# Optimization experiments

Hardware: AMD Instinct MI355X
Metric: run time of the kernel (lower is better)

## Reference

```python
import jax, jax.numpy as jnp
import numpy as np


def setup_inputs() -> dict:
    key = jax.random.key(0)
    ks = jax.random.split(key, 12)
    B, N, D_in, D = 64, 512, 512, 512
    inp = {
        "x": jax.random.normal(ks[0], (B, N, D_in), dtype=jnp.float32),
        "adj": jax.random.uniform(ks[1], (B, N, N), dtype=jnp.float32),
        "mask": jnp.ones((B, N, 1), dtype=jnp.float32),
        "W_enc": jax.random.normal(ks[2], (D_in, D), dtype=jnp.float32) * (1.0 / np.sqrt(D_in)),
        "b_enc": jnp.zeros((D,), dtype=jnp.float32),
        "Wz": jax.random.normal(ks[3], (D, D), dtype=jnp.float32) * (1.0 / np.sqrt(D)),
        "Uz": jax.random.normal(ks[4], (D, D), dtype=jnp.float32) * (1.0 / np.sqrt(D)),
        "bz": jnp.zeros((D,), dtype=jnp.float32),
        "Wr": jax.random.normal(ks[5], (D, D), dtype=jnp.float32) * (1.0 / np.sqrt(D)),
        "Ur": jax.random.normal(ks[6], (D, D), dtype=jnp.float32) * (1.0 / np.sqrt(D)),
        "br": jnp.zeros((D,), dtype=jnp.float32),
        "Wh": jax.random.normal(ks[7], (D, D), dtype=jnp.float32) * (1.0 / np.sqrt(D)),
        "Uh": jax.random.normal(ks[8], (D, D), dtype=jnp.float32) * (1.0 / np.sqrt(D)),
        "bh": jnp.zeros((D,), dtype=jnp.float32),
        "ba": jnp.zeros((D,), dtype=jnp.float32),
        "steps": 2,
    }
    return inp


def _gru_step(h, adj, mask, Wz, Uz, bz, Wr, Ur, br, Wh, Uh, bh, ba, act):
    # aggregated neighbor messages: [B,N,D]
    a = jnp.einsum('bnm,bmd->bnd', adj, h) + ba
    z = act(a @ Wz + h @ Uz + bz)          # update gate
    r = act(a @ Wr + h @ Ur + br)          # reset gate
    hc = jnp.tanh(a @ Wh + (r * h) @ Uh + bh)
    hc = hc * mask
    return (1.0 - z) * h + z * hc


def reference(x, adj, mask, W_enc, b_enc, Wz, Uz, bz, Wr, Ur, br, Wh, Uh, bh, ba, steps):
    act = jax.nn.relu
    h = mask * act(x @ W_enc + b_enc)      # [B,N,D]
    for _ in range(steps):
        h = _gru_step(h, adj, mask, Wz, Uz, bz, Wr, Ur, br, Wh, Uh, bh, ba, act)
    return h
```

## Files before the change

kernel.cpp:

```cpp
#include <hip/hip_runtime.h>


#define LD 512
#define NN ((long)LD * LD)

typedef unsigned short u16;
typedef _Float16 f16;
typedef f16 f16x8 __attribute__((ext_vector_type(8)));
typedef float f32x4 __attribute__((ext_vector_type(4)));

__device__ __forceinline__ u16 f2h(float f) { f16 h = (f16)f; return *(u16*)&h; }
__device__ __forceinline__ float h2f(u16 b) { f16 h = *(f16*)&b; return (float)h; }

__device__ __forceinline__ void gload16(const void* g, void* l) {
  __builtin_amdgcn_global_load_lds(
      (const __attribute__((address_space(1))) void*)g,
      (__attribute__((address_space(3))) void*)l, 16, 0, 0);
}

__global__ void cvt_f16(const float* __restrict__ in, u16* __restrict__ out, int n4) {
  int i = blockIdx.x * blockDim.x + threadIdx.x;
  if (i >= n4) return;
  float4 v = reinterpret_cast<const float4*>(in)[i];
  ushort4 o;
  o.x = f2h(v.x); o.y = f2h(v.y); o.z = f2h(v.z); o.w = f2h(v.w);
  reinterpret_cast<ushort4*>(out)[i] = o;
}

__global__ void cvt2h(const float* __restrict__ in, u16* __restrict__ ohi,
                      u16* __restrict__ olo, int n4) {
  int i = blockIdx.x * blockDim.x + threadIdx.x;
  if (i >= n4) return;
  float4 v = reinterpret_cast<const float4*>(in)[i];
  ushort4 h, l;
  h.x = f2h(v.x); l.x = f2h(v.x - h2f(h.x));
  h.y = f2h(v.y); l.y = f2h(v.y - h2f(h.y));
  h.z = f2h(v.z); l.z = f2h(v.z - h2f(h.z));
  h.w = f2h(v.w); l.w = f2h(v.w - h2f(h.w));
  reinterpret_cast<ushort4*>(ohi)[i] = h;
  reinterpret_cast<ushort4*>(olo)[i] = l;
}

__global__ void wconv1(const float* __restrict__ in, u16* __restrict__ out, float scale) {
  __shared__ float sm[32][33];
  int tx = threadIdx.x & 31, ty = threadIdx.x >> 5;
  int k0 = blockIdx.y * 32, n0 = blockIdx.x * 32;
#pragma unroll
  for (int i = 0; i < 32; i += 8)
    sm[ty + i][tx] = in[(size_t)(k0 + ty + i) * LD + n0 + tx];
  __syncthreads();
#pragma unroll
  for (int i = 0; i < 32; i += 8)
    out[(size_t)(n0 + ty + i) * LD + k0 + tx] = f2h(sm[tx][ty + i] * scale);
}

__global__ void wconv2h(const float* __restrict__ in, u16* __restrict__ ohi,
                        u16* __restrict__ olo, float scale) {
  __shared__ float sm[32][33];
  int tx = threadIdx.x & 31, ty = threadIdx.x >> 5;
  int k0 = blockIdx.y * 32, n0 = blockIdx.x * 32;
#pragma unroll
  for (int i = 0; i < 32; i += 8)
    sm[ty + i][tx] = in[(size_t)(k0 + ty + i) * LD + n0 + tx];
  __syncthreads();
#pragma unroll
  for (int i = 0; i < 32; i += 8) {
    float v = sm[tx][ty + i] * scale;
    u16 hi = f2h(v);
    size_t o = (size_t)(n0 + ty + i) * LD + k0 + tx;
    ohi[o] = hi;
    olo[o] = f2h(v - h2f(hi));
  }
}

__global__ void transp16(const u16* __restrict__ in, u16* __restrict__ out) {
  __shared__ u16 sm[64][65];
  int b = blockIdx.z;
  int n0 = blockIdx.y * 64, d0 = blockIdx.x * 64;
  int lane = threadIdx.x & 63, grp = threadIdx.x >> 6;
  const u16* src = in + ((size_t)b * LD + n0) * LD + d0;
#pragma unroll
  for (int i = grp; i < 64; i += 4)
    sm[i][lane] = src[(size_t)i * LD + lane];
  __syncthreads();
  u16* dst = out + ((size_t)b * LD + d0) * LD + n0;
#pragma unroll
  for (int i = grp; i < 64; i += 4)
    dst[(size_t)i * LD + lane] = sm[lane][i];
}

struct PENC {
  static constexpr int P = 3;
  static constexpr int AI[3] = {0, 1, 1}, BI[3] = {0, 0, 1};
  static constexpr int SA[3] = {1, 1, 0}, SB[3] = {1, 0, 1};
};
struct PA {
  static constexpr int P = 1;
  static constexpr int AI[1] = {0}, BI[1] = {0};
  static constexpr int SA[1] = {1}, SB[1] = {1};
};
struct PZ {
  static constexpr int P = 2;
  static constexpr int AI[2] = {0, 1}, BI[2] = {0, 1};
  static constexpr int SA[2] = {1, 1}, SB[2] = {1, 1};
};
struct PR {
  static constexpr int P = 4;
  static constexpr int AI[4] = {0, 0, 1, 2}, BI[4] = {0, 1, 1, 2};
  static constexpr int SA[4] = {1, 0, 1, 1}, SB[4] = {1, 1, 0, 1};
};
struct PG1 {
  static constexpr int P = 6;
  static constexpr int AI[6] = {0, 0, 1, 2, 3, 3}, BI[6] = {0, 1, 1, 2, 2, 3};
  static constexpr int SA[6] = {1, 0, 1, 1, 1, 0}, SB[6] = {1, 1, 0, 1, 0, 1};
};
struct PG2 {
  static constexpr int P = 2;
  static constexpr int AI[2] = {0, 1}, BI[2] = {0, 1};
  static constexpr int SA[2] = {1, 1}, SB[2] = {1, 1};
};

struct Desc {
  const u16* Aop[4];
  const u16* Bop[4];
  const float* bias1;
  const float* mask;
  const float* hf32;
  const u16* z16;
  float* outf;
  u16* o16;
  u16* o16b;
};

template <int EPI, class PL>
__global__ __launch_bounds__(512, 4) void gemmf(Desc d) {
  __shared__ __align__(16) u16 As[2][8192];
  __shared__ __align__(16) u16 Bs[2][4096];

  const int t = threadIdx.x;
  const int lane = t & 63;
  const int wid = t >> 6;
  const int wr = wid >> 1, wc = wid & 1;

  const int id = (int)blockIdx.x;
  const int swz = (id & 7) * 64 + (id >> 3);
  const int colb = swz & 3;
  const int rowb = swz >> 2;
  size_t baseA, baseB;
  int rowBase0;
  if (EPI == 1) {
    const int by2 = rowb & 1;
    const size_t bz = (size_t)(rowb >> 1);
    baseA = bz * NN + (size_t)by2 * 256 * LD;
    baseB = bz * NN + (size_t)colb * 128 * LD;
    rowBase0 = (int)bz * 512 + by2 * 256;
  } else {
    baseA = (size_t)rowb * 256 * LD;
    baseB = (size_t)colb * 128 * LD;
    rowBase0 = rowb * 256;
  }

  auto stageA = [&](const u16* Aop, int kb, u16* dst) {
#pragma unroll
    for (int s = 0; s < 2; ++s) {
      const int r = s * 128 + (t >> 2), c = t & 3;
      const int g = c ^ (r & 3) ^ ((r >> 2) & 3);
      gload16(Aop + baseA + (size_t)r * LD + kb + g * 8, dst + s * 4096 + t * 8);
    }
  };
  auto stageB = [&](const u16* Bop, int kb, u16* dst) {
    const int r = t >> 2, c = t & 3;
    const int g = c ^ (r & 3) ^ ((r >> 2) & 3);
    gload16(Bop + baseB + (size_t)r * LD + kb + g * 8, dst + t * 8);
  };

  const int lk = lane >> 4;
  const int RA = wr * 64 + (lane & 15);
  const int RB = wc * 64 + (lane & 15);
  const int offA = RA * 32 + ((lk ^ ((RA & 3) ^ ((RA >> 2) & 3))) * 8);
  const int offB = RB * 32 + ((lk ^ ((RB & 3) ^ ((RB >> 2) & 3))) * 8);

  f32x4 acc[4][4] = {};

  stageA(d.Aop[PL::AI[0]], 0, As[0]);
  stageB(d.Bop[PL::BI[0]], 0, Bs[0]);
  asm volatile("s_waitcnt vmcnt(0)" ::: "memory");
  __builtin_amdgcn_s_barrier();

  int aS = 0, bS = 0;
  for (int kk = 0; kk < 16; ++kk) {
#pragma unroll
    for (int p = 0; p < PL::P; ++p) {
      f16x8 af[4], bf[4];
#pragma unroll
      for (int i = 0; i < 4; ++i) af[i] = *(const f16x8*)&As[aS][offA + i * 512];
#pragma unroll
      for (int j = 0; j < 4; ++j) bf[j] = *(const f16x8*)&Bs[bS][offB + j * 512];
      const int np = (p + 1 == PL::P) ? 0 : p + 1;
      const int nkb = (p + 1 == PL::P) ? (kk + 1) * 32 : kk * 32;
      const bool last = (kk == 15) && (p == PL::P - 1);
      if (!last) {
        if (PL::SA[np]) stageA(d.Aop[PL::AI[np]], nkb, As[aS ^ 1]);
        if (PL::SB[np]) stageB(d.Bop[PL::BI[np]], nkb, Bs[bS ^ 1]);
      }
      __builtin_amdgcn_s_setprio(1);
#pragma unroll
      for (int i = 0; i < 4; ++i)
#pragma unroll
        for (int j = 0; j < 4; ++j)
          acc[i][j] = __builtin_amdgcn_mfma_f32_16x16x32_f16(af[i], bf[j], acc[i][j], 0, 0, 0);
      __builtin_amdgcn_s_setprio(0);
      __syncthreads();
      if (!last) {
        aS ^= PL::SA[np];
        bS ^= PL::SB[np];
      }
    }
  }

  const float S4 = 0.0625f;
  const float S12 = 2.44140625e-4f;
  const int rowBase = rowBase0 + wr * 64 + (lane >> 4) * 4;
  const int colBase = colb * 128 + wc * 64 + (lane & 15);
#pragma unroll
  for (int i = 0; i < 4; ++i) {
#pragma unroll
    for (int j = 0; j < 4; ++j) {
      const int col = colBase + j * 16;
      const float bv = d.bias1[col];
#pragma unroll
      for (int r = 0; r < 4; ++r) {
        const int row = rowBase + i * 16 + r;
        const size_t idx = (size_t)row * LD + col;
        const float a = acc[i][j][r];
        if (EPI == 0) {
          float v = fmaxf(a + bv, 0.0f) * d.mask[row];
          d.outf[idx] = v;
          d.o16[idx] = f2h(v * S4);
        } else if (EPI == 1) {
          float v = a + bv * S4;
          u16 hi = f2h(v);
          d.o16[idx] = hi;
          d.o16b[idx] = f2h(v - h2f(hi));
        } else if (EPI == 2) {
          float v = fmaxf(a + bv, 0.0f);
          d.o16[idx] = f2h(v * S4);
        } else if (EPI == 3) {
          float v = fmaxf(a + bv, 0.0f) * d.hf32[idx];
          u16 hi = f2h(v * S12);
          d.o16[idx] = hi;
          float rec = h2f(hi) * 4096.0f;
          d.o16b[idx] = f2h((v - rec) * S12);
        } else {
          float hc = tanhf(a + bv) * d.mask[row];
          float z = 16.0f * h2f(d.z16[idx]);
          float h = d.hf32[idx];
          float hn = (1.0f - z) * h + z * hc;
          d.outf[idx] = hn;
          d.o16[idx] = f2h(hn * S4);
        }
      }
    }
  }
}

extern "C" void kernel_launch(void* const* d_in, const int* in_sizes, int n_in,
                              void* d_out, int out_size, void* d_ws, size_t ws_size,
                              hipStream_t stream) {
  const float* x    = (const float*)d_in[0];
  const float* adj  = (const float*)d_in[1];
  const float* mask = (const float*)d_in[2];
  const float* Wenc = (const float*)d_in[3];
  const float* benc = (const float*)d_in[4];
  const float* Wz   = (const float*)d_in[5];
  const float* Uz   = (const float*)d_in[6];
  const float* bz_  = (const float*)d_in[7];
  const float* Wr   = (const float*)d_in[8];
  const float* Ur   = (const float*)d_in[9];
  const float* br_  = (const float*)d_in[10];
  const float* Wh   = (const float*)d_in[11];
  const float* Uh   = (const float*)d_in[12];
  const float* bh_  = (const float*)d_in[13];
  const float* ba_  = (const float*)d_in[14];

  float* hf = (float*)d_out;

  const size_t SZ  = (size_t)64 * 512 * 512 * sizeof(u16);
  const size_t WSZ = (size_t)LD * LD * sizeof(u16);
  const size_t NEED = 7 * SZ + 11 * WSZ;
  if (ws_size < NEED) return;

  char* p = (char*)d_ws;
  u16* adj16 = (u16*)p; p += SZ;
  u16* h16   = (u16*)p; p += SZ;
  u16* a_hi  = (u16*)p; p += SZ;
  u16* a_lo  = (u16*)p; p += SZ;
  u16* zht   = (u16*)p; p += SZ;
  u16* rh_hi = (u16*)p; p += SZ;
  u16* rh_lo = (u16*)p; p += SZ;
  u16* w     = (u16*)p;
  u16* We_h = w + 0 * LD * LD;  u16* We_l = w + 1 * LD * LD;
  u16* Wz1  = w + 2 * LD * LD;
  u16* Uz1  = w + 3 * LD * LD;
  u16* Wr_h = w + 4 * LD * LD;  u16* Wr_l = w + 5 * LD * LD;
  u16* Ur1  = w + 6 * LD * LD;
  u16* Wh_h = w + 7 * LD * LD;  u16* Wh_l = w + 8 * LD * LD;
  u16* Uh_h = w + 9 * LD * LD;  u16* Uh_l = w + 10 * LD * LD;
  u16* x_hi = a_hi;
  u16* x_lo = a_lo;

  const int NELT = 64 * 512 * 512;
  cvt2h<<<NELT / 4 / 256, 256, 0, stream>>>(x, x_hi, x_lo, NELT / 4);
  cvt_f16<<<NELT / 4 / 256, 256, 0, stream>>>(adj, adj16, NELT / 4);

  dim3 wg(16, 16);
  wconv2h<<<wg, 256, 0, stream>>>(Wenc, We_h, We_l, 1.0f);
  wconv1<<<wg, 256, 0, stream>>>(Wz, Wz1, 16.0f);
  wconv1<<<wg, 256, 0, stream>>>(Uz, Uz1, 16.0f);
  wconv2h<<<wg, 256, 0, stream>>>(Wr, Wr_h, Wr_l, 16.0f);
  wconv1<<<wg, 256, 0, stream>>>(Ur, Ur1, 16.0f);
  wconv2h<<<wg, 256, 0, stream>>>(Wh, Wh_h, Wh_l, 16.0f);
  wconv2h<<<wg, 256, 0, stream>>>(Uh, Uh_h, Uh_l, 4096.0f);

  {
    Desc d{};
    d.Aop[0] = x_lo; d.Aop[1] = x_hi;
    d.Bop[0] = We_h; d.Bop[1] = We_l;
    d.bias1 = benc; d.mask = mask; d.outf = hf; d.o16 = h16;
    gemmf<0, PENC><<<512, 512, 0, stream>>>(d);
  }

  for (int s = 0; s < 2; ++s) {
    transp16<<<dim3(8, 8, 64), 256, 0, stream>>>(h16, zht);
    {
      Desc d{};
      d.Aop[0] = adj16; d.Bop[0] = zht;
      d.bias1 = ba_; d.o16 = a_hi; d.o16b = a_lo;
      gemmf<1, PA><<<512, 512, 0, stream>>>(d);
    }
    {
      Desc d{};
      d.Aop[0] = a_hi; d.Aop[1] = h16;
      d.Bop[0] = Wz1;  d.Bop[1] = Uz1;
      d.bias1 = bz_; d.o16 = zht;
      gemmf<2, PZ><<<512, 512, 0, stream>>>(d);
    }
    {
      Desc d{};
      d.Aop[0] = a_hi; d.Aop[1] = a_lo; d.Aop[2] = h16;
      d.Bop[0] = Wr_l; d.Bop[1] = Wr_h; d.Bop[2] = Ur1;
      d.bias1 = br_; d.hf32 = hf; d.o16 = rh_hi; d.o16b = rh_lo;
      gemmf<3, PR><<<512, 512, 0, stream>>>(d);
    }
    if (s == 0) {
      Desc d{};
      d.Aop[0] = a_hi; d.Aop[1] = a_lo; d.Aop[2] = rh_lo; d.Aop[3] = rh_hi;
      d.Bop[0] = Wh_l; d.Bop[1] = Wh_h; d.Bop[2] = Uh_h;  d.Bop[3] = Uh_l;
      d.bias1 = bh_; d.mask = mask; d.hf32 = hf; d.z16 = zht;
      d.outf = hf; d.o16 = h16;
      gemmf<4, PG1><<<512, 512, 0, stream>>>(d);
    } else {
      Desc d{};
      d.Aop[0] = a_hi; d.Aop[1] = rh_hi;
      d.Bop[0] = Wh_h; d.Bop[1] = Uh_h;
      d.bias1 = bh_; d.mask = mask; d.hf32 = hf; d.z16 = zht;
      d.outf = hf; d.o16 = h16;
      gemmf<4, PG2><<<512, 512, 0, stream>>>(d);
    }
  }
}
```

Baseline: 765.1 us.

## Fuse z-gate GEMM into candidate GEMM, widen tiles, triple-buffer LDS

Removes the separate z-gate GEMM pass. The z accumulation now happens in a second accumulator set inside the final candidate/update kernel, with z computed in the epilogue, so zht is no longer written and re-read. Block tiles grow from 256x128 to 256x256 with half as many blocks, and the LDS pipeline moves from double buffering with a full syncthreads to a 3-slot ring with vmcnt-based waits, prefetching two stages ahead. In exchange, register pressure rises (up to 2x4x8 accumulators) and occupancy is lowered to 2 waves per SIMD via launch bounds.

Measured after the change: 1.677 ms. 2.19x slower.

```diff
diff --git a/kernel.cpp b/kernel.cpp
--- a/kernel.cpp
+++ b/kernel.cpp
@@ -2,7 +2,9 @@
 
 
 #define LD 512
-#define NN ((long)LD * LD)
+#define NNL ((long)LD * LD)
+#define BARRIER do { asm volatile("s_barrier" ::: "memory"); \
+                     __builtin_amdgcn_sched_barrier(0); } while (0)
 
 typedef unsigned short u16;
 typedef _Float16 f16;
@@ -16,6 +18,12 @@
   __builtin_amdgcn_global_load_lds(
       (const __attribute__((address_space(1))) void*)g,
       (__attribute__((address_space(3))) void*)l, 16, 0, 0);
+}
+
+__device__ __forceinline__ void vwaitN(int n) {
+  if (n == 4)      asm volatile("s_waitcnt vmcnt(4)" ::: "memory");
+  else if (n == 2) asm volatile("s_waitcnt vmcnt(2)" ::: "memory");
+  else             asm volatile("s_waitcnt vmcnt(0)" ::: "memory");
 }
 
 __global__ void cvt_f16(const float* __restrict__ in, u16* __restrict__ out, int n4) {
@@ -89,53 +97,55 @@
     dst[(size_t)i * LD + lane] = sm[lane][i];
 }
 
-struct PENC {
-  static constexpr int P = 3;
-  static constexpr int AI[3] = {0, 1, 1}, BI[3] = {0, 0, 1};
+struct LENC {
+  enum { P = 3, NACC = 1 };
+  static constexpr int AI[3] = {0, 1, 1}, BI[3] = {0, 0, 1}, AC[3] = {0, 0, 0};
   static constexpr int SA[3] = {1, 1, 0}, SB[3] = {1, 0, 1};
 };
-struct PA {
-  static constexpr int P = 1;
-  static constexpr int AI[1] = {0}, BI[1] = {0};
+struct LA {
+  enum { P = 1, NACC = 1 };
+  static constexpr int AI[1] = {0}, BI[1] = {0}, AC[1] = {0};
   static constexpr int SA[1] = {1}, SB[1] = {1};
 };
-struct PZ {
-  static constexpr int P = 2;
-  static constexpr int AI[2] = {0, 1}, BI[2] = {0, 1};
-  static constexpr int SA[2] = {1, 1}, SB[2] = {1, 1};
-};
-struct PR {
-  static constexpr int P = 4;
-  static constexpr int AI[4] = {0, 0, 1, 2}, BI[4] = {0, 1, 1, 2};
+struct LR {
+  enum { P = 4, NACC = 1 };
+  static constexpr int AI[4] = {0, 0, 1, 2}, BI[4] = {0, 1, 1, 2}, AC[4] = {0, 0, 0, 0};
   static constexpr int SA[4] = {1, 0, 1, 1}, SB[4] = {1, 1, 0, 1};
 };
-struct PG1 {
-  static constexpr int P = 6;
-  static constexpr int AI[6] = {0, 0, 1, 2, 3, 3}, BI[6] = {0, 1, 1, 2, 2, 3};
-  static constexpr int SA[6] = {1, 0, 1, 1, 1, 0}, SB[6] = {1, 1, 0, 1, 0, 1};
-};
-struct PG2 {
-  static constexpr int P = 2;
-  static constexpr int AI[2] = {0, 1}, BI[2] = {0, 1};
-  static constexpr int SA[2] = {1, 1}, SB[2] = {1, 1};
+struct LZG1 {
+  enum { P = 8, NACC = 2 };
+  static constexpr int AI[8] = {0, 0, 0, 1, 2, 3, 3, 4};
+  static constexpr int BI[8] = {0, 1, 2, 2, 3, 3, 4, 5};
+  static constexpr int AC[8] = {1, 0, 0, 0, 0, 0, 0, 1};
+  static constexpr int SA[8] = {1, 0, 0, 1, 1, 1, 0, 1};
+  static constexpr int SB[8] = {1, 1, 1, 0, 1, 0, 1, 1};
+};
+struct LZG2 {
+  enum { P = 4, NACC = 2 };
+  static constexpr int AI[4] = {0, 0, 1, 2}, BI[4] = {0, 1, 2, 3};
+  static constexpr int AC[4] = {1, 0, 0, 1};
+  static constexpr int SA[4] = {1, 0, 1, 1}, SB[4] = {1, 1, 1, 1};
 };
 
 struct Desc {
-  const u16* Aop[4];
-  const u16* Bop[4];
-  const float* bias1;
+  const u16* Aop[5];
+  const u16* Bop[6];
+  const float* biasG;
+  const float* biasZ;
   const float* mask;
   const float* hf32;
-  const u16* z16;
   float* outf;
   u16* o16;
   u16* o16b;
 };
 
 template <int EPI, class PL>
-__global__ __launch_bounds__(512, 4) void gemmf(Desc d) {
-  __shared__ __align__(16) u16 As[2][8192];
-  __shared__ __align__(16) u16 Bs[2][4096];
+__global__ __launch_bounds__(512, 2) void gemmz(Desc d) {
+  constexpr int P = PL::P;
+  constexpr int NQ = 16 * P;
+
+  __shared__ __align__(16) u16 Aring[3 * 8192];
+  __shared__ __align__(16) u16 Bring[3 * 8192];
 
   const int t = threadIdx.x;
   const int lane = t & 63;
@@ -143,96 +153,110 @@
   const int wr = wid >> 1, wc = wid & 1;
 
   const int id = (int)blockIdx.x;
-  const int swz = (id & 7) * 64 + (id >> 3);
-  const int colb = swz & 3;
-  const int rowb = swz >> 2;
+  const int swz = (id & 7) * 32 + (id >> 3);
+  const int colb = swz & 1;
+  const int rowb = swz >> 1;
   size_t baseA, baseB;
   int rowBase0;
   if (EPI == 1) {
-    const int by2 = rowb & 1;
     const size_t bz = (size_t)(rowb >> 1);
-    baseA = bz * NN + (size_t)by2 * 256 * LD;
-    baseB = bz * NN + (size_t)colb * 128 * LD;
-    rowBase0 = (int)bz * 512 + by2 * 256;
+    baseA = bz * NNL + (size_t)(rowb & 1) * 256 * LD;
+    baseB = bz * NNL + (size_t)colb * 256 * LD;
+    rowBase0 = (int)bz * 512 + (rowb & 1) * 256;
   } else {
     baseA = (size_t)rowb * 256 * LD;
-    baseB = (size_t)colb * 128 * LD;
+    baseB = (size_t)colb * 256 * LD;
     rowBase0 = rowb * 256;
   }
 
-  auto stageA = [&](const u16* Aop, int kb, u16* dst) {
-#pragma unroll
-    for (int s = 0; s < 2; ++s) {
-      const int r = s * 128 + (t >> 2), c = t & 3;
-      const int g = c ^ (r & 3) ^ ((r >> 2) & 3);
-      gload16(Aop + baseA + (size_t)r * LD + kb + g * 8, dst + s * 4096 + t * 8);
+  auto stA = [&](const u16* op, int kb, int slot) {
+#pragma unroll
+    for (int k = 0; k < 2; ++k) {
+      const int c = t + 512 * k, r = c >> 2;
+      const int g = (c & 3) ^ ((r & 3) ^ ((r >> 2) & 3));
+      gload16(op + baseA + (size_t)r * LD + kb + g * 8, Aring + slot * 8192 + c * 8);
     }
   };
-  auto stageB = [&](const u16* Bop, int kb, u16* dst) {
-    const int r = t >> 2, c = t & 3;
-    const int g = c ^ (r & 3) ^ ((r >> 2) & 3);
-    gload16(Bop + baseB + (size_t)r * LD + kb + g * 8, dst + t * 8);
+  auto stB = [&](const u16* op, int kb, int slot) {
+#pragma unroll
+    for (int k = 0; k < 2; ++k) {
+      const int c = t + 512 * k, r = c >> 2;
+      const int g = (c & 3) ^ ((r & 3) ^ ((r >> 2) & 3));
+      gload16(op + baseB + (size_t)r * LD + kb + g * 8, Bring + slot * 8192 + c * 8);
+    }
   };
 
   const int lk = lane >> 4;
   const int RA = wr * 64 + (lane & 15);
-  const int RB = wc * 64 + (lane & 15);
-  const int offA = RA * 32 + ((lk ^ ((RA & 3) ^ ((RA >> 2) & 3))) * 8);
-  const int offB = RB * 32 + ((lk ^ ((RB & 3) ^ ((RB >> 2) & 3))) * 8);
-
-  f32x4 acc[4][4] = {};
-
-  stageA(d.Aop[PL::AI[0]], 0, As[0]);
-  stageB(d.Bop[PL::BI[0]], 0, Bs[0]);
-  asm volatile("s_waitcnt vmcnt(0)" ::: "memory");
-  __builtin_amdgcn_s_barrier();
-
-  int aS = 0, bS = 0;
+  const int RB = wc * 128 + (lane & 15);
+  const int aoff = RA * 32 + ((lk ^ ((RA & 3) ^ ((RA >> 2) & 3))) * 8);
+  const int boff = RB * 32 + ((lk ^ ((RB & 3) ^ ((RB >> 2) & 3))) * 8);
+
+  f32x4 acc[PL::NACC][4][8] = {};
+
+  stA(d.Aop[PL::AI[0]], 0, 0);
+  stB(d.Bop[PL::BI[0]], 0, 0);
+  {
+    constexpr int p1c = 1 % P;
+    constexpr int kb1 = (1 / P) * 32;
+    if (PL::SA[p1c]) stA(d.Aop[PL::AI[p1c]], kb1, 1);
+    if (PL::SB[p1c]) stB(d.Bop[PL::BI[p1c]], kb1, 1);
+    vwaitN(2 * (PL::SA[p1c] + PL::SB[p1c]));
+  }
+  BARRIER;
+
+  int rA = 0, rB = 0;
   for (int kk = 0; kk < 16; ++kk) {
 #pragma unroll
-    for (int p = 0; p < PL::P; ++p) {
-      f16x8 af[4], bf[4];
-#pragma unroll
-      for (int i = 0; i < 4; ++i) af[i] = *(const f16x8*)&As[aS][offA + i * 512];
-#pragma unroll
-      for (int j = 0; j < 4; ++j) bf[j] = *(const f16x8*)&Bs[bS][offB + j * 512];
-      const int np = (p + 1 == PL::P) ? 0 : p + 1;
-      const int nkb = (p + 1 == PL::P) ? (kk + 1) * 32 : kk * 32;
-      const bool last = (kk == 15) && (p == PL::P - 1);
-      if (!last) {
-        if (PL::SA[np]) stageA(d.Aop[PL::AI[np]], nkb, As[aS ^ 1]);
-        if (PL::SB[np]) stageB(d.Bop[PL::BI[np]], nkb, Bs[bS ^ 1]);
+    for (int p = 0; p < P; ++p) {
+      const int q = kk * P + p;
+      const int p1 = (p + 1) % P, p2 = (p + 2) % P;
+      const int kb2 = (p + 2 < P) ? kk * 32 : (p + 2 < 2 * P) ? (kk + 1) * 32 : (kk + 2) * 32;
+      const bool st2 = (q + 2) < NQ;
+
+      f16x8 af[4], bf[8];
+      {
+        const u16* As_ = Aring + rA * 8192;
+        const u16* Bs_ = Bring + rB * 8192;
+#pragma unroll
+        for (int i = 0; i < 4; ++i) af[i] = *(const f16x8*)&As_[aoff + i * 512];
+#pragma unroll
+        for (int j = 0; j < 8; ++j) bf[j] = *(const f16x8*)&Bs_[boff + j * 512];
+      }
+      if (st2) {
+        if (PL::SA[p2]) stA(d.Aop[PL::AI[p2]], kb2, (rA + PL::SA[p1] + 1) % 3);
+        if (PL::SB[p2]) stB(d.Bop[PL::BI[p2]], kb2, (rB + PL::SB[p1] + 1) % 3);
       }
       __builtin_amdgcn_s_setprio(1);
+      const int n = PL::AC[p];
 #pragma unroll
       for (int i = 0; i < 4; ++i)
 #pragma unroll
-        for (int j = 0; j < 4; ++j)
-          acc[i][j] = __builtin_amdgcn_mfma_f32_16x16x32_f16(af[i], bf[j], acc[i][j], 0, 0, 0);
+        for (int j = 0; j < 8; ++j)
+          acc[n][i][j] = __builtin_amdgcn_mfma_f32_16x16x32_f16(af[i], bf[j], acc[n][i][j], 0, 0, 0);
       __builtin_amdgcn_s_setprio(0);
-      __syncthreads();
-      if (!last) {
-        aS ^= PL::SA[np];
-        bS ^= PL::SB[np];
-      }
+      vwaitN(st2 ? 2 * (PL::SA[p2] + PL::SB[p2]) : 0);
+      BARRIER;
+      rA = (rA + PL::SA[p1]) % 3;
+      rB = (rB + PL::SB[p1]) % 3;
     }
   }
 
   const float S4 = 0.0625f;
   const float S12 = 2.44140625e-4f;
   const int rowBase = rowBase0 + wr * 64 + (lane >> 4) * 4;
-  const int colBase = colb * 128 + wc * 64 + (lane & 15);
+  const int colBase = colb * 256 + wc * 128 + (lane & 15);
 #pragma unroll
   for (int i = 0; i < 4; ++i) {
 #pragma unroll
-    for (int j = 0; j < 4; ++j) {
+    for (int j = 0; j < 8; ++j) {
       const int col = colBase + j * 16;
-      const float bv = d.bias1[col];
+      const float bv = d.biasG[col];
 #pragma unroll
       for (int r = 0; r < 4; ++r) {
         const int row = rowBase + i * 16 + r;
         const size_t idx = (size_t)row * LD + col;
-        const float a = acc[i][j][r];
+        const float a = acc[0][i][j][r];
         if (EPI == 0) {
           float v = fmaxf(a + bv, 0.0f) * d.mask[row];
           d.outf[idx] = v;
@@ -242,9 +266,6 @@
           u16 hi = f2h(v);
           d.o16[idx] = hi;
           d.o16b[idx] = f2h(v - h2f(hi));
-        } else if (EPI == 2) {
-          float v = fmaxf(a + bv, 0.0f);
-          d.o16[idx] = f2h(v * S4);
         } else if (EPI == 3) {
           float v = fmaxf(a + bv, 0.0f) * d.hf32[idx];
           u16 hi = f2h(v * S12);
@@ -252,8 +273,9 @@
           float rec = h2f(hi) * 4096.0f;
           d.o16b[idx] = f2h((v - rec) * S12);
         } else {
+          float vz = fmaxf(acc[PL::NACC - 1][i][j][r] + d.biasZ[col], 0.0f);
+          float z = 16.0f * h2f(f2h(vz * S4));
           float hc = tanhf(a + bv) * d.mask[row];
-          float z = 16.0f * h2f(d.z16[idx]);
           float h = d.hf32[idx];
           float hn = (1.0f - z) * h + z * hc;
           d.outf[idx] = hn;
@@ -295,7 +317,7 @@
   u16* h16   = (u16*)p; p += SZ;
   u16* a_hi  = (u16*)p; p += SZ;
   u16* a_lo  = (u16*)p; p += SZ;
-  u16* zht   = (u16*)p; p += SZ;
+  u16* ht16  = (u16*)p; p += SZ;
   u16* rh_hi = (u16*)p; p += SZ;
   u16* rh_lo = (u16*)p; p += SZ;
   u16* w     = (u16*)p;
@@ -326,46 +348,40 @@
     Desc d{};
     d.Aop[0] = x_lo; d.Aop[1] = x_hi;
     d.Bop[0] = We_h; d.Bop[1] = We_l;
-    d.bias1 = benc; d.mask = mask; d.outf = hf; d.o16 = h16;
-    gemmf<0, PENC><<<512, 512, 0, stream>>>(d);
+    d.biasG = benc; d.mask = mask; d.outf = hf; d.o16 = h16;
+    gemmz<0, LENC><<<256, 512, 0, stream>>>(d);
   }
 
   for (int s = 0; s < 2; ++s) {
-    transp16<<<dim3(8, 8, 64), 256, 0, stream>>>(h16, zht);
+    transp16<<<dim3(8, 8, 64), 256, 0, stream>>>(h16, ht16);
     {
       Desc d{};
-      d.Aop[0] = adj16; d.Bop[0] = zht;
-      d.bias1 = ba_; d.o16 = a_hi; d.o16b = a_lo;
-      gemmf<1, PA><<<512, 512, 0, stream>>>(d);
-    }
-    {
-      Desc d{};
-      d.Aop[0] = a_hi; d.Aop[1] = h16;
-      d.Bop[0] = Wz1;  d.Bop[1] = Uz1;
-      d.bias1 = bz_; d.o16 = zht;
-      gemmf<2, PZ><<<512, 512, 0, stream>>>(d);
+      d.Aop[0] = adj16; d.Bop[0] = ht16;
+      d.biasG = ba_; d.o16 = a_hi; d.o16b = a_lo;
+      gemmz<1, LA><<<256, 512, 0, stream>>>(d);
     }
     {
       Desc d{};
       d.Aop[0] = a_hi; d.Aop[1] = a_lo; d.Aop[2] = h16;
       d.Bop[0] = Wr_l; d.Bop[1] = Wr_h; d.Bop[2] = Ur1;
-      d.bias1 = br_; d.hf32 = hf; d.o16 = rh_hi; d.o16b = rh_lo;
-      gemmf<3, PR><<<512, 512, 0, stream>>>(d);
+      d.biasG = br_; d.hf32 = hf; d.o16 = rh_hi; d.o16b = rh_lo;
+      gemmz<3, LR><<<256, 512, 0, stream>>>(d);
     }
     if (s == 0) {
       Desc d{};
-      d.Aop[0] = a_hi; d.Aop[1] = a_lo; d.Aop[2] = rh_lo; d.Aop[3] = rh_hi;
-      d.Bop[0] = Wh_l; d.Bop[1] = Wh_h; d.Bop[2] = Uh_h;  d.Bop[3] = Uh_l;
-      d.bias1 = bh_; d.mask = mask; d.hf32 = hf; d.z16 = zht;
+      d.Aop[0] = a_hi; d.Aop[1] = a_lo; d.Aop[2] = rh_lo; d.Aop[3] = rh_hi; d.Aop[4] = h16;
+      d.Bop[0] = Wz1;  d.Bop[1] = Wh_l; d.Bop[2] = Wh_h;  d.Bop[3] = Uh_h;
+      d.Bop[4] = Uh_l; d.Bop[5] = Uz1;
+      d.biasG = bh_; d.biasZ = bz_; d.mask = mask; d.hf32 = hf;
       d.outf = hf; d.o16 = h16;
-      gemmf<4, PG1><<<512, 512, 0, stream>>>(d);
+      gemmz<5, LZG1><<<256, 512, 0, stream>>>(d);
     } else {
       Desc d{};
-      d.Aop[0] = a_hi; d.Aop[1] = rh_hi;
-      d.Bop[0] = Wh_h; d.Bop[1] = Uh_h;
-      d.bias1 = bh_; d.mask = mask; d.hf32 = hf; d.z16 = zht;
+      d.Aop[0] = a_hi; d.Aop[1] = rh_hi; d.Aop[2] = h16;
+      d.Bop[0] = Wz1;  d.Bop[1] = Wh_h;  d.Bop[2] = Uh_h; d.Bop[3] = Uz1;
+      d.biasG = bh_; d.biasZ = bz_; d.mask = mask; d.hf32 = hf;
       d.outf = hf; d.o16 = h16;
-      gemmf<4, PG2><<<512, 512, 0, stream>>>(d);
-    }
-  }
-}
+      gemmz<5, LZG2><<<256, 512, 0, stream>>>(d);
+    }
+  }
+}
```
